# Optimization experiments

Hardware: AMD Instinct MI355X
Metric: run time of the kernel (lower is better)

The kernel has to match this reference:

```python
import jax, jax.numpy as jnp
import numpy as np

N, E = 50000, 1600000
F_IN, F_EDGE, HID = 128, 16, 64
SLOPE = 0.2
EPS_BN = 1e-5


def setup_inputs() -> dict:
    key = jax.random.key(0)
    ks = jax.random.split(key, 24)
    g = lambda k, shp, s=0.1: (jax.random.normal(k, shp, dtype=jnp.float32) * s)
    inp = {
        'x': jax.random.normal(ks[0], (N, F_IN), dtype=jnp.float32),
        'edge_index': jax.random.randint(ks[1], (2, E), 0, N, dtype=jnp.int64),
        'edge_attr': jax.random.normal(ks[2], (E, F_EDGE), dtype=jnp.float32),
        # conv1: F_IN -> HID, 4 heads, concat
        'W1': g(ks[3], (F_IN, 4 * HID)), 'a1s': g(ks[4], (4, HID)), 'a1d': g(ks[5], (4, HID)), 'b1': jnp.zeros((4 * HID,), jnp.float32),
        # conv2: 4*HID -> HID, 4 heads, concat
        'W2': g(ks[6], (4 * HID, 4 * HID)), 'a2s': g(ks[7], (4, HID)), 'a2d': g(ks[8], (4, HID)), 'b2': jnp.zeros((4 * HID,), jnp.float32),
        # conv3: 4*HID -> HID, 1 head
        'W3': g(ks[9], (4 * HID, HID)), 'a3s': g(ks[10], (1, HID)), 'a3d': g(ks[11], (1, HID)), 'b3': jnp.zeros((HID,), jnp.float32),
        'bn1_g': jnp.ones((4 * HID,), jnp.float32), 'bn1_b': jnp.zeros((4 * HID,), jnp.float32),
        'bn2_g': jnp.ones((4 * HID,), jnp.float32), 'bn2_b': jnp.zeros((4 * HID,), jnp.float32),
        'mlp_W1': g(ks[12], (F_EDGE, HID)), 'mlp_b1': jnp.zeros((HID,), jnp.float32),
        'mlp_W2': g(ks[13], (HID, HID)), 'mlp_b2': jnp.zeros((HID,), jnp.float32),
        'fc_W': g(ks[14], (3 * HID, 1)), 'fc_b': jnp.zeros((1,), jnp.float32),
    }
    return inp


def _gat(x, W, a_s, a_d, b, src, dst, heads, dout):
    n = x.shape[0]
    h = (x @ W).reshape(n, heads, dout)                    # [N,H,D]
    ls = jnp.sum(h * a_s, axis=-1)                         # [N,H]
    ld = jnp.sum(h * a_d, axis=-1)
    logits = jax.nn.leaky_relu(ls[src] + ld[dst], SLOPE)   # [E',H]
    m = jax.ops.segment_max(logits, dst, num_segments=n)
    m = jnp.where(jnp.isfinite(m), m, 0.0)
    p = jnp.exp(logits - m[dst])
    s = jax.ops.segment_sum(p, dst, num_segments=n)
    alpha = p / (s[dst] + 1e-16)                           # segment softmax over in-edges
    out = jax.ops.segment_sum(h[src] * alpha[:, :, None], dst, num_segments=n)
    return out.reshape(n, heads * dout) + b


def _bn(x, g, b):
    mu = jnp.mean(x, axis=0)
    var = jnp.var(x, axis=0)
    return (x - mu) * jax.lax.rsqrt(var + EPS_BN) * g + b


def reference(x, edge_index, edge_attr, W1, a1s, a1d, b1, W2, a2s, a2d, b2,
              W3, a3s, a3d, b3, bn1_g, bn1_b, bn2_g, bn2_b,
              mlp_W1, mlp_b1, mlp_W2, mlp_b2, fc_W, fc_b):
    src0, dst0 = edge_index[0], edge_index[1]
    loop = jnp.arange(x.shape[0], dtype=edge_index.dtype)  # PyG adds self-loops
    src = jnp.concatenate([src0, loop])
    dst = jnp.concatenate([dst0, loop])

    h = _gat(x, W1, a1s, a1d, b1, src, dst, 4, HID)
    h = _bn(jax.nn.elu(h), bn1_g, bn1_b)
    h = _gat(h, W2, a2s, a2d, b2, src, dst, 4, HID)
    h = _bn(jax.nn.elu(h), bn2_g, bn2_b)
    h = _gat(h, W3, a3s, a3d, b3, src, dst, 1, HID)        # [N,HID]

    ef = jax.nn.relu(edge_attr @ mlp_W1 + mlp_b1) @ mlp_W2 + mlp_b2  # [E,HID]
    emb = jnp.concatenate([h[src0], h[dst0], ef], axis=1)  # [E,3*HID]
    return (emb @ fc_W + fc_b).squeeze(-1)
```

## Files before the change

### kernel.cpp

```cpp
#include <hip/hip_runtime.h>
#include <math.h>


#define FIN 128
#define HID 64
#define BIN_SHIFT 8

typedef __bf16 bf16x8 __attribute__((ext_vector_type(8)));
typedef float f32x4 __attribute__((ext_vector_type(4)));

__device__ __forceinline__ unsigned f2bfbits(float f) {
    unsigned u = __float_as_uint(f);
    return (u + 0x7fffu + ((u >> 16) & 1u)) >> 16;
}
__device__ __forceinline__ float bf_lo(unsigned w) { return __uint_as_float(w << 16); }
__device__ __forceinline__ float bf_hi(unsigned w) { return __uint_as_float(w & 0xffff0000u); }
__device__ __forceinline__ float bf1(unsigned short s) { return __uint_as_float(((unsigned)s) << 16); }

__device__ __forceinline__ unsigned fenc(float f) {
    unsigned b = __float_as_uint(f);
    return (b & 0x80000000u) ? ~b : (b | 0x80000000u);
}
__device__ __forceinline__ float fdec(unsigned k) {
    unsigned b = (k & 0x80000000u) ? (k ^ 0x80000000u) : ~k;
    return __uint_as_float(b);
}


__global__ __launch_bounds__(256) void bincount_kernel(const int* __restrict__ ei,
                                                       int* __restrict__ bincnt,
                                                       int E, int Etot) {
    __shared__ int h[256];
    int t = threadIdx.x;
    h[t] = 0;
    __syncthreads();
    int base = blockIdx.x * 4096;
    #pragma unroll
    for (int i = 0; i < 16; ++i) {
        int e = base + i * 256 + t;
        if (e < Etot) {
            int d = (e < E) ? ei[E + e] : (e - E);
            atomicAdd(&h[d >> BIN_SHIFT], 1);
        }
    }
    __syncthreads();
    if (h[t]) atomicAdd(&bincnt[t], h[t]);
}

__global__ void scanbins_kernel(const int* __restrict__ bincnt, int* __restrict__ binptr,
                                int* __restrict__ bincur, int NB, int Etot) {
    __shared__ int buf[256];
    int t = threadIdx.x;
    int v = (t < NB) ? bincnt[t] : 0;
    buf[t] = v;
    __syncthreads();
    for (int o = 1; o < 256; o <<= 1) {
        int y = (t >= o) ? buf[t - o] : 0;
        __syncthreads();
        buf[t] += y;
        __syncthreads();
    }
    int excl = buf[t] - v;
    if (t < NB) {
        binptr[t] = excl;
        bincur[t] = excl;
    }
    if (t == 0) binptr[NB] = Etot;
}

__global__ __launch_bounds__(256) void binscatter_kernel(const int* __restrict__ ei,
                                                         int* __restrict__ bincur,
                                                         int2* __restrict__ binned,
                                                         int E, int Etot) {
    __shared__ int h[256];
    __shared__ int gb[256];
    int t = threadIdx.x;
    h[t] = 0;
    __syncthreads();
    int base = blockIdx.x * 4096;
    #pragma unroll
    for (int i = 0; i < 16; ++i) {
        int e = base + i * 256 + t;
        if (e < Etot) {
            int d = (e < E) ? ei[E + e] : (e - E);
            atomicAdd(&h[d >> BIN_SHIFT], 1);
        }
    }
    __syncthreads();
    int cnt = h[t];
    if (cnt) gb[t] = atomicAdd(&bincur[t], cnt);
    __syncthreads();
    h[t] = 0;
    __syncthreads();
    #pragma unroll
    for (int i = 0; i < 16; ++i) {
        int e = base + i * 256 + t;
        if (e < Etot) {
            int s, d;
            if (e < E) { s = ei[e]; d = ei[E + e]; }
            else       { s = e - E; d = e - E; }
            int b = d >> BIN_SHIFT;
            int pos = gb[b] + atomicAdd(&h[b], 1);
            binned[pos] = make_int2(s, d);
        }
    }
}

__global__ __launch_bounds__(256) void bincsr_kernel(const int2* __restrict__ binned,
                                                     const int* __restrict__ binptr,
                                                     int* __restrict__ row_ptr,
                                                     int* __restrict__ col,
                                                     int N, int Etot) {
    __shared__ int h[256];
    __shared__ int cur[256];
    __shared__ int wsum[4];
    int b = blockIdx.x;
    int t = threadIdx.x;
    int lo = b << BIN_SHIFT;
    h[t] = 0;
    __syncthreads();
    int ebeg = binptr[b], eend = binptr[b + 1];
    for (int i = ebeg + t; i < eend; i += 256) atomicAdd(&h[binned[i].y - lo], 1);
    __syncthreads();
    int v = h[t];
    int lane = t & 63, w = t >> 6;
    int x = v;
    #pragma unroll
    for (int o = 1; o < 64; o <<= 1) {
        int y = __shfl_up(x, o);
        if (lane >= o) x += y;
    }
    if (lane == 63) wsum[w] = x;
    __syncthreads();
    int off = 0;
    #pragma unroll
    for (int i = 0; i < 4; ++i) off += (i < w) ? wsum[i] : 0;
    int excl = ebeg + off + x - v;
    int node = lo + t;
    if (node < N) row_ptr[node] = excl;
    cur[t] = excl;
    if (b == 0 && t == 0) row_ptr[N] = Etot;
    __syncthreads();
    for (int i = ebeg + t; i < eend; i += 256) {
        int2 sd = binned[i];
        int pos = atomicAdd(&cur[sd.y - lo], 1);
        col[pos] = sd.x;
    }
}


__global__ __launch_bounds__(256) void mfma_gemm_kernel(
    const float* __restrict__ X, const float* __restrict__ W,
    unsigned short* __restrict__ Yb, int Nrows, int K, int M,
    const float* __restrict__ scale, const float* __restrict__ shift) {
    __shared__ __align__(16) unsigned short a_lds[128][40];
    __shared__ __align__(16) unsigned short b_lds[64][40];
    const int t = threadIdx.x;
    const int row0 = blockIdx.x * 128;
    const int c0 = blockIdx.y * 64;
    const int w = t >> 6, lane = t & 63;
    const int quad = lane >> 4, mrow = lane & 15;
    f32x4 acc[2][4] = {};
    for (int k0 = 0; k0 < K; k0 += 32) {
        #pragma unroll
        for (int i = 0; i < 4; ++i) {
            int f = i * 256 + t;
            int r = f >> 3, kq = f & 7;
            int grow = row0 + r;
            float4 xv = make_float4(0.f, 0.f, 0.f, 0.f);
            if (grow < Nrows) xv = *(const float4*)(X + (size_t)grow * K + k0 + kq * 4);
            if (scale) {
                float4 sc = *(const float4*)(scale + k0 + kq * 4);
                float4 sh = *(const float4*)(shift + k0 + kq * 4);
                xv.x = fmaf(xv.x, sc.x, sh.x);
                xv.y = fmaf(xv.y, sc.y, sh.y);
                xv.z = fmaf(xv.z, sc.z, sh.z);
                xv.w = fmaf(xv.w, sc.w, sh.w);
            }
            ushort4 pk;
            pk.x = (unsigned short)f2bfbits(xv.x);
            pk.y = (unsigned short)f2bfbits(xv.y);
            pk.z = (unsigned short)f2bfbits(xv.z);
            pk.w = (unsigned short)f2bfbits(xv.w);
            *(ushort4*)&a_lds[r][kq * 4] = pk;
        }
        #pragma unroll
        for (int i = 0; i < 2; ++i) {
            int f = i * 256 + t;
            int kr = f >> 4, cq = f & 15;
            float4 wv = *(const float4*)(W + (size_t)(k0 + kr) * M + c0 + cq * 4);
            b_lds[cq * 4 + 0][kr] = (unsigned short)f2bfbits(wv.x);
            b_lds[cq * 4 + 1][kr] = (unsigned short)f2bfbits(wv.y);
            b_lds[cq * 4 + 2][kr] = (unsigned short)f2bfbits(wv.z);
            b_lds[cq * 4 + 3][kr] = (unsigned short)f2bfbits(wv.w);
        }
        __syncthreads();
        bf16x8 a0 = *(const bf16x8*)&a_lds[w * 32 + mrow][quad * 8];
        bf16x8 a1 = *(const bf16x8*)&a_lds[w * 32 + 16 + mrow][quad * 8];
        #pragma unroll
        for (int c = 0; c < 4; ++c) {
            bf16x8 bf = *(const bf16x8*)&b_lds[c * 16 + mrow][quad * 8];
            acc[0][c] = __builtin_amdgcn_mfma_f32_16x16x32_bf16(a0, bf, acc[0][c], 0, 0, 0);
            acc[1][c] = __builtin_amdgcn_mfma_f32_16x16x32_bf16(a1, bf, acc[1][c], 0, 0, 0);
        }
        __syncthreads();
    }
    #pragma unroll
    for (int i = 0; i < 2; ++i) {
        #pragma unroll
        for (int c = 0; c < 4; ++c) {
            #pragma unroll
            for (int r = 0; r < 4; ++r) {
                int grow = row0 + w * 32 + i * 16 + quad * 4 + r;
                if (grow < Nrows)
                    Yb[(size_t)grow * M + c0 + c * 16 + mrow] =
                        (unsigned short)f2bfbits(acc[i][c][r]);
            }
        }
    }
}


template <int H>
__global__ __launch_bounds__(256) void attn_coef_kernel(
    const unsigned short* __restrict__ hb, const float* __restrict__ as_,
    const float* __restrict__ ad_, float* __restrict__ ls,
    float* __restrict__ ld, unsigned* __restrict__ lsmax_g, int N, int ngroups) {
    __shared__ unsigned lmax_lds[4];
    int t = threadIdx.x;
    if (t < 4) lmax_lds[t] = 0;
    __syncthreads();
    int lane = t & 63;
    float lmax = -3.0e38f;
    for (int g = blockIdx.x; g < ngroups; g += gridDim.x) {
        int n = g * 4 + (t >> 6);
        if (n >= N) continue;
        if (H == 4) {
            uint2 w = *(const uint2*)(hb + (size_t)n * 256 + lane * 4);
            float h0 = bf_lo(w.x), h1 = bf_hi(w.x), h2 = bf_lo(w.y), h3 = bf_hi(w.y);
            int cg = lane * 4;
            float4 av = *(const float4*)(as_ + cg);
            float4 dv = *(const float4*)(ad_ + cg);
            float su = h0 * av.x + h1 * av.y + h2 * av.z + h3 * av.w;
            float sd = h0 * dv.x + h1 * dv.y + h2 * dv.z + h3 * dv.w;
            #pragma unroll
            for (int o = 1; o < 16; o <<= 1) {
                su += __shfl_xor(su, o);
                sd += __shfl_xor(sd, o);
            }
            if ((lane & 15) == 0) {
                int hd = lane >> 4;
                ls[(size_t)n * 4 + hd] = su;
                ld[(size_t)n * 4 + hd] = sd;
            }
            lmax = fmaxf(lmax, su);
        } else {
            float hv = bf1(hb[(size_t)n * 64 + lane]);
            float su = hv * as_[lane];
            float sd = hv * ad_[lane];
            #pragma unroll
            for (int o = 32; o; o >>= 1) {
                su += __shfl_xor(su, o);
                sd += __shfl_xor(sd, o);
            }
            if (lane == 0) {
                ls[n] = su;
                ld[n] = sd;
            }
            lmax = fmaxf(lmax, su);
        }
    }
    unsigned key = fenc(lmax);
    if (H == 4) {
        if ((lane & 15) == 0) atomicMax(&lmax_lds[lane >> 4], key);
    } else {
        if (lane == 0) atomicMax(&lmax_lds[0], key);
    }
    __syncthreads();
    if (t < H) atomicMax(&lsmax_g[t], lmax_lds[t]);
}


__global__ __launch_bounds__(256) void agg4_kernel(
    const unsigned short* __restrict__ hb, const float* __restrict__ ls,
    const float* __restrict__ ld, const int* __restrict__ row_ptr,
    const int* __restrict__ col, const float* __restrict__ bias,
    const unsigned* __restrict__ lsmax_g, float* __restrict__ out, int N) {
    int lane = threadIdx.x & 63;
    int n = blockIdx.x * 4 + (threadIdx.x >> 6);
    if (n >= N) return;
    int beg = row_ptr[n], end = row_ptr[n + 1];
    const int hd = lane >> 4;
    float4 ldn = *(const float4*)(ld + (size_t)n * 4);
    float ldn_h = (hd == 0) ? ldn.x : (hd == 1) ? ldn.y : (hd == 2) ? ldn.z : ldn.w;
    float m_h = fmaxf(0.f, ldn_h + fdec(lsmax_g[hd]));
    const int c0 = lane * 4;
    float psum = 0.f;
    float a0 = 0.f, a1 = 0.f, a2 = 0.f, a3 = 0.f;
    for (int base = beg; base < end; base += 64) {
        int el = base + lane;
        int s_r = (el < end) ? col[el] : 0;
        int cnt = min(64, end - base);
        int j = 0;
        for (; j + 8 <= cnt; j += 8) {
            int s[8];
            float l[8];
            uint2 w[8];
            #pragma unroll
            for (int q = 0; q < 8; ++q) s[q] = __shfl(s_r, j + q);
            #pragma unroll
            for (int q = 0; q < 8; ++q) l[q] = ls[(size_t)s[q] * 4 + hd];
            #pragma unroll
            for (int q = 0; q < 8; ++q) w[q] = *(const uint2*)(hb + (size_t)s[q] * 256 + c0);
            #pragma unroll
            for (int q = 0; q < 8; ++q) {
                float g = l[q] + ldn_h;
                g = fmaxf(g, 0.2f * g);
                float p = __expf(g - m_h);
                psum += p;
                a0 = fmaf(p, bf_lo(w[q].x), a0);
                a1 = fmaf(p, bf_hi(w[q].x), a1);
                a2 = fmaf(p, bf_lo(w[q].y), a2);
                a3 = fmaf(p, bf_hi(w[q].y), a3);
            }
        }
        for (; j < cnt; ++j) {
            int sj = __shfl(s_r, j);
            float lv = ls[(size_t)sj * 4 + hd];
            float gg = lv + ldn_h;
            gg = fmaxf(gg, 0.2f * gg);
            float pv = __expf(gg - m_h);
            psum += pv;
            uint2 w = *(const uint2*)(hb + (size_t)sj * 256 + c0);
            a0 = fmaf(pv, bf_lo(w.x), a0);
            a1 = fmaf(pv, bf_hi(w.x), a1);
            a2 = fmaf(pv, bf_lo(w.y), a2);
            a3 = fmaf(pv, bf_hi(w.y), a3);
        }
    }
    float inv = 1.f / (psum + 1e-16f);
    float4 bv = *(const float4*)(bias + c0);
    float4 o;
    o.x = fmaf(a0, inv, bv.x);
    o.y = fmaf(a1, inv, bv.y);
    o.z = fmaf(a2, inv, bv.z);
    o.w = fmaf(a3, inv, bv.w);
    o.x = (o.x > 0.f) ? o.x : expm1f(o.x);
    o.y = (o.y > 0.f) ? o.y : expm1f(o.y);
    o.z = (o.z > 0.f) ? o.z : expm1f(o.z);
    o.w = (o.w > 0.f) ? o.w : expm1f(o.w);
    *(float4*)(out + (size_t)n * 256 + c0) = o;
}


__global__ __launch_bounds__(256) void agg3_kernel(
    const unsigned short* __restrict__ hb, const float* __restrict__ ls,
    const float* __restrict__ ld, const int* __restrict__ row_ptr,
    const int* __restrict__ col, const float* __restrict__ bias,
    const float* __restrict__ fcW, float* __restrict__ up, float* __restrict__ vp,
    const unsigned* __restrict__ lsmax_g, int N) {
    int lane = threadIdx.x & 63;
    int n = blockIdx.x * 4 + (threadIdx.x >> 6);
    if (n >= N) return;
    int beg = row_ptr[n], end = row_ptr[n + 1];
    float ldn = ld[n];
    float m_h = fmaxf(0.f, ldn + fdec(lsmax_g[0]));
    int g = lane >> 4;
    int li = lane & 15;
    float psum = 0.f;
    float a0 = 0.f, a1 = 0.f, a2 = 0.f, a3 = 0.f;
    for (int j = beg + g; j < end; j += 4) {
        int s = col[j];
        float lg = ls[s] + ldn;
        lg = fmaxf(lg, 0.2f * lg);
        float pv = __expf(lg - m_h);
        psum += pv;
        uint2 w = *(const uint2*)(hb + (size_t)s * 64 + li * 4);
        a0 = fmaf(pv, bf_lo(w.x), a0);
        a1 = fmaf(pv, bf_hi(w.x), a1);
        a2 = fmaf(pv, bf_lo(w.y), a2);
        a3 = fmaf(pv, bf_hi(w.y), a3);
    }
    #pragma unroll
    for (int o = 16; o <= 32; o <<= 1) {
        psum += __shfl_xor(psum, o);
        a0 += __shfl_xor(a0, o);
        a1 += __shfl_xor(a1, o);
        a2 += __shfl_xor(a2, o);
        a3 += __shfl_xor(a3, o);
    }
    float inv = 1.f / (psum + 1e-16f);
    int c = li * 4;
    float v0 = fmaf(a0, inv, bias[c + 0]);
    float v1 = fmaf(a1, inv, bias[c + 1]);
    float v2 = fmaf(a2, inv, bias[c + 2]);
    float v3 = fmaf(a3, inv, bias[c + 3]);
    float pu = v0 * fcW[c] + v1 * fcW[c + 1] + v2 * fcW[c + 2] + v3 * fcW[c + 3];
    float pv2 = v0 * fcW[64 + c] + v1 * fcW[64 + c + 1] + v2 * fcW[64 + c + 2] +
                v3 * fcW[64 + c + 3];
    #pragma unroll
    for (int o = 1; o <= 8; o <<= 1) {
        pu += __shfl_xor(pu, o);
        pv2 += __shfl_xor(pv2, o);
    }
    if (lane == 0) {
        up[n] = pu;
        vp[n] = pv2;
    }
}


__global__ __launch_bounds__(256) void bn_stats_kernel(const float* __restrict__ y,
                                                       float* __restrict__ sums,
                                                       int N) {
    int c = threadIdx.x;
    int r0 = blockIdx.x * 128;
    int rend = min(r0 + 128, N);
    float s = 0.f, s2 = 0.f;
    for (int r = r0; r < rend; ++r) {
        float v = y[(size_t)r * 256 + c];
        s += v;
        s2 += v * v;
    }
    atomicAdd(&sums[c], s);
    atomicAdd(&sums[256 + c], s2);
}

__global__ void bn_finalize_kernel(const float* __restrict__ sums,
                                   const float* __restrict__ g,
                                   const float* __restrict__ b,
                                   float* __restrict__ scale,
                                   float* __restrict__ shift, int N) {
    int c = threadIdx.x;
    float invN = 1.f / (float)N;
    float mu = sums[c] * invN;
    float var = sums[256 + c] * invN - mu * mu;
    float sc = g[c] * rsqrtf(var + 1e-5f);
    scale[c] = sc;
    shift[c] = b[c] - mu * sc;
}


__global__ void prep_kernel(const float* __restrict__ mlpW2,
                            const float* __restrict__ mlpb2,
                            const float* __restrict__ fcW,
                            const float* __restrict__ fcb,
                            float* __restrict__ w2f, float* __restrict__ c2) {
    int j = threadIdx.x;
    float s = 0.f;
    for (int k = 0; k < 64; ++k) s += mlpW2[j * 64 + k] * fcW[128 + k];
    w2f[j] = s;
    if (j == 0) {
        float c = fcb[0];
        for (int k = 0; k < 64; ++k) c += mlpb2[k] * fcW[128 + k];
        c2[0] = c;
    }
}

__global__ __launch_bounds__(256) void edge_out_kernel(
    const int* __restrict__ ei, const float* __restrict__ ea,
    const float* __restrict__ W1, const float* __restrict__ b1,
    const float* __restrict__ w2f, const float* __restrict__ c2p,
    const float* __restrict__ u, const float* __restrict__ v,
    float* __restrict__ out, int E) {
    __shared__ __align__(16) float W1T[64][16];
    __shared__ float w2fl[64];
    __shared__ float b1l[64];
    int t = threadIdx.x;
    for (int p = t; p < 1024; p += 256) {
        int i = p >> 6, j = p & 63;
        W1T[j][i] = W1[i * 64 + j];
    }
    if (t < 64) {
        w2fl[t] = w2f[t];
        b1l[t] = b1[t];
    }
    __syncthreads();
    int base = blockIdx.x * 1024;
    float eav[4][16];
    int sidx[4], didx[4];
    bool ok[4];
    #pragma unroll
    for (int k = 0; k < 4; ++k) {
        int e = base + k * 256 + t;
        ok[k] = e < E;
        int ec = ok[k] ? e : 0;
        sidx[k] = ei[ec];
        didx[k] = ei[E + ec];
        const float4* ear = (const float4*)(ea + (size_t)ec * 16);
        float4 q0 = ear[0], q1 = ear[1], q2 = ear[2], q3 = ear[3];
        eav[k][0] = q0.x;  eav[k][1] = q0.y;  eav[k][2] = q0.z;  eav[k][3] = q0.w;
        eav[k][4] = q1.x;  eav[k][5] = q1.y;  eav[k][6] = q1.z;  eav[k][7] = q1.w;
        eav[k][8] = q2.x;  eav[k][9] = q2.y;  eav[k][10] = q2.z; eav[k][11] = q2.w;
        eav[k][12] = q3.x; eav[k][13] = q3.y; eav[k][14] = q3.z; eav[k][15] = q3.w;
    }
    float acc[4] = {0.f, 0.f, 0.f, 0.f};
    #pragma unroll 4
    for (int j = 0; j < 64; ++j) {
        const float4* wr = (const float4*)&W1T[j][0];
        float4 w0 = wr[0], w1 = wr[1], w2 = wr[2], w3 = wr[3];
        float wrow[16] = {w0.x, w0.y, w0.z, w0.w, w1.x, w1.y, w1.z, w1.w,
                          w2.x, w2.y, w2.z, w2.w, w3.x, w3.y, w3.z, w3.w};
        float bj = b1l[j], wj = w2fl[j];
        #pragma unroll
        for (int k = 0; k < 4; ++k) {
            float s = bj;
            #pragma unroll
            for (int q = 0; q < 16; ++q) s = fmaf(eav[k][q], wrow[q], s);
            s = fmaxf(s, 0.f);
            acc[k] = fmaf(s, wj, acc[k]);
        }
    }
    float cc = c2p[0];
    #pragma unroll
    for (int k = 0; k < 4; ++k) {
        if (ok[k]) {
            int e = base + k * 256 + t;
            out[e] = u[sidx[k]] + v[didx[k]] + acc[k] + cc;
        }
    }
}


extern "C" void kernel_launch(void* const* d_in, const int* in_sizes, int n_in,
                              void* d_out, int out_size, void* d_ws, size_t ws_size,
                              hipStream_t stream) {
    const float* x     = (const float*)d_in[0];
    const int*   ei    = (const int*)d_in[1];
    const float* ea    = (const float*)d_in[2];
    const float* W1    = (const float*)d_in[3];
    const float* a1s   = (const float*)d_in[4];
    const float* a1d   = (const float*)d_in[5];
    const float* b1    = (const float*)d_in[6];
    const float* W2    = (const float*)d_in[7];
    const float* a2s   = (const float*)d_in[8];
    const float* a2d   = (const float*)d_in[9];
    const float* b2    = (const float*)d_in[10];
    const float* W3    = (const float*)d_in[11];
    const float* a3s   = (const float*)d_in[12];
    const float* a3d   = (const float*)d_in[13];
    const float* b3    = (const float*)d_in[14];
    const float* bn1g  = (const float*)d_in[15];
    const float* bn1b  = (const float*)d_in[16];
    const float* bn2g  = (const float*)d_in[17];
    const float* bn2b  = (const float*)d_in[18];
    const float* mlpW1 = (const float*)d_in[19];
    const float* mlpb1 = (const float*)d_in[20];
    const float* mlpW2 = (const float*)d_in[21];
    const float* mlpb2 = (const float*)d_in[22];
    const float* fcW   = (const float*)d_in[23];
    const float* fcb   = (const float*)d_in[24];
    float* out = (float*)d_out;

    const int N = in_sizes[0] / FIN;
    const int E = in_sizes[1] / 2;
    const int Etot = E + N;
    const int NB = (N + 255) >> BIN_SHIFT;

    char* wsb = (char*)d_ws;
    size_t off = 0;
    auto alloc = [&](size_t bytes) {
        void* p = wsb + off;
        off += (bytes + 63) & ~(size_t)63;
        return p;
    };
    unsigned short* hAb = (unsigned short*)alloc((size_t)N * 256 * 2);
    float* hB  = (float*)alloc((size_t)N * 256 * 4);
    unsigned short* h3b = (unsigned short*)alloc((size_t)N * 64 * 2);
    float* lsb = (float*)alloc((size_t)N * 4 * 4);
    float* ldb = (float*)alloc((size_t)N * 4 * 4);
    int* row_ptr = (int*)alloc((size_t)(N + 1) * 4);
    int* colb    = (int*)alloc((size_t)Etot * 4);
    int2* binned = (int2*)alloc((size_t)Etot * 8);
    int* bincnt  = (int*)alloc(256 * 4 + 12 * 4);
    unsigned* lsmax1 = (unsigned*)(bincnt + 256);
    unsigned* lsmax2 = lsmax1 + 4;
    unsigned* lsmax3 = lsmax1 + 8;
    int* binptr  = (int*)alloc((size_t)(NB + 1) * 4);
    int* bincur  = (int*)alloc((size_t)NB * 4);
    float* bnsum   = (float*)alloc(512 * 4);
    float* bnscale = (float*)alloc(256 * 4);
    float* bnshift = (float*)alloc(256 * 4);
    float* ub  = (float*)alloc((size_t)N * 4);
    float* vb  = (float*)alloc((size_t)N * 4);
    float* w2f = (float*)alloc(64 * 4);
    float* c2  = (float*)alloc(16 * 4);
    (void)ws_size; (void)n_in; (void)out_size;

    const int nb4 = (N + 3) / 4;
    const int nch = (Etot + 4095) / 4096;

    hipMemsetAsync(bincnt, 0, (256 + 12) * sizeof(int), stream);
    bincount_kernel<<<nch, 256, 0, stream>>>(ei, bincnt, E, Etot);
    scanbins_kernel<<<1, 256, 0, stream>>>(bincnt, binptr, bincur, NB, Etot);
    binscatter_kernel<<<nch, 256, 0, stream>>>(ei, bincur, binned, E, Etot);
    bincsr_kernel<<<NB, 256, 0, stream>>>(binned, binptr, row_ptr, colb, N, Etot);

    dim3 ggrid((N + 127) / 128, 4);
    dim3 ggrid3((N + 127) / 128, 1);

    mfma_gemm_kernel<<<ggrid, 256, 0, stream>>>(x, W1, hAb, N, 128, 256, nullptr, nullptr);
    attn_coef_kernel<4><<<2048, 256, 0, stream>>>(hAb, a1s, a1d, lsb, ldb, lsmax1, N, nb4);
    agg4_kernel<<<nb4, 256, 0, stream>>>(hAb, lsb, ldb, row_ptr, colb, b1, lsmax1, hB, N);
    hipMemsetAsync(bnsum, 0, 512 * sizeof(float), stream);
    bn_stats_kernel<<<(N + 127) / 128, 256, 0, stream>>>(hB, bnsum, N);
    bn_finalize_kernel<<<1, 256, 0, stream>>>(bnsum, bn1g, bn1b, bnscale, bnshift, N);

    mfma_gemm_kernel<<<ggrid, 256, 0, stream>>>(hB, W2, hAb, N, 256, 256, bnscale, bnshift);
    attn_coef_kernel<4><<<2048, 256, 0, stream>>>(hAb, a2s, a2d, lsb, ldb, lsmax2, N, nb4);
    agg4_kernel<<<nb4, 256, 0, stream>>>(hAb, lsb, ldb, row_ptr, colb, b2, lsmax2, hB, N);
    hipMemsetAsync(bnsum, 0, 512 * sizeof(float), stream);
    bn_stats_kernel<<<(N + 127) / 128, 256, 0, stream>>>(hB, bnsum, N);
    bn_finalize_kernel<<<1, 256, 0, stream>>>(bnsum, bn2g, bn2b, bnscale, bnshift, N);

    mfma_gemm_kernel<<<ggrid3, 256, 0, stream>>>(hB, W3, h3b, N, 256, 64, bnscale, bnshift);
    attn_coef_kernel<1><<<2048, 256, 0, stream>>>(h3b, a3s, a3d, lsb, ldb, lsmax3, N, nb4);
    agg3_kernel<<<nb4, 256, 0, stream>>>(h3b, lsb, ldb, row_ptr, colb, b3,
                                         fcW, ub, vb, lsmax3, N);

    prep_kernel<<<1, 64, 0, stream>>>(mlpW2, mlpb2, fcW, fcb, w2f, c2);
    edge_out_kernel<<<(E + 1023) / 1024, 256, 0, stream>>>(ei, ea, mlpW1, mlpb1, w2f, c2,
                                                           ub, vb, out, E);
}
```

Measured before the change: 866.0 us.

## Fuse attention coefs into GEMM epilogue, BN stats into aggregation, switch to fp16

The attention logit dot products now run in the GEMM epilogue, computed from the accumulators with shuffles, so the separate attn_coef pass is gone. The aggregation kernel becomes persistent and accumulates BN sums and squares in shared memory, which removes the bn_stats pass over hB. BN finalize moves into the next GEMM's prologue, and the prep kernel folds into edge_out. Storage and MFMA switch from bf16 to fp16. This cuts launches and full-tensor reads, at the cost of fp16 range risk and a shallower unroll in the gather loop (8 to 4).

```diff
diff --git a/kernel.cpp b/kernel.cpp
--- a/kernel.cpp
+++ b/kernel.cpp
@@ -1,4 +1,5 @@
 #include <hip/hip_runtime.h>
+#include <hip/hip_fp16.h>
 #include <math.h>
 
 
@@ -6,16 +7,17 @@
 #define HID 64
 #define BIN_SHIFT 8
 
-typedef __bf16 bf16x8 __attribute__((ext_vector_type(8)));
+typedef _Float16 f16x8 __attribute__((ext_vector_type(8)));
 typedef float f32x4 __attribute__((ext_vector_type(4)));
 
-__device__ __forceinline__ unsigned f2bfbits(float f) {
-    unsigned u = __float_as_uint(f);
-    return (u + 0x7fffu + ((u >> 16) & 1u)) >> 16;
-}
-__device__ __forceinline__ float bf_lo(unsigned w) { return __uint_as_float(w << 16); }
-__device__ __forceinline__ float bf_hi(unsigned w) { return __uint_as_float(w & 0xffff0000u); }
-__device__ __forceinline__ float bf1(unsigned short s) { return __uint_as_float(((unsigned)s) << 16); }
+__device__ __forceinline__ unsigned short f2hbits(float f) {
+    __half h = __float2half(f);
+    return *reinterpret_cast<unsigned short*>(&h);
+}
+__device__ __forceinline__ float2 hpair(unsigned w) {
+    __half2 h = *reinterpret_cast<__half2*>(&w);
+    return __half22float2(h);
+}
 
 __device__ __forceinline__ unsigned fenc(float f) {
     unsigned b = __float_as_uint(f);
@@ -151,15 +153,32 @@
 
 __global__ __launch_bounds__(256) void mfma_gemm_kernel(
     const float* __restrict__ X, const float* __restrict__ W,
-    unsigned short* __restrict__ Yb, int Nrows, int K, int M,
-    const float* __restrict__ scale, const float* __restrict__ shift) {
+    unsigned short* __restrict__ Yh, int Nrows, int K, int M,
+    const float* __restrict__ bnsum, const float* __restrict__ bng,
+    const float* __restrict__ bnb, float invN,
+    const float* __restrict__ as_, const float* __restrict__ ad_,
+    float* __restrict__ ls, float* __restrict__ ld,
+    unsigned* __restrict__ lsmax_g, int H) {
     __shared__ __align__(16) unsigned short a_lds[128][40];
     __shared__ __align__(16) unsigned short b_lds[64][40];
+    __shared__ __align__(16) float scale_l[256];
+    __shared__ __align__(16) float shift_l[256];
+    __shared__ unsigned lmax_l;
     const int t = threadIdx.x;
     const int row0 = blockIdx.x * 128;
-    const int c0 = blockIdx.y * 64;
+    const int by = blockIdx.y;
+    const int c0 = by * 64;
     const int w = t >> 6, lane = t & 63;
     const int quad = lane >> 4, mrow = lane & 15;
+    if (t == 0) lmax_l = 0;
+    if (bnsum && t < 256) {
+        float mu = bnsum[t] * invN;
+        float var = bnsum[256 + t] * invN - mu * mu;
+        float sc = bng[t] * rsqrtf(var + 1e-5f);
+        scale_l[t] = sc;
+        shift_l[t] = bnb[t] - mu * sc;
+    }
+    __syncthreads();
     f32x4 acc[2][4] = {};
     for (int k0 = 0; k0 < K; k0 += 32) {
         #pragma unroll
@@ -169,19 +188,19 @@
             int grow = row0 + r;
             float4 xv = make_float4(0.f, 0.f, 0.f, 0.f);
             if (grow < Nrows) xv = *(const float4*)(X + (size_t)grow * K + k0 + kq * 4);
-            if (scale) {
-                float4 sc = *(const float4*)(scale + k0 + kq * 4);
-                float4 sh = *(const float4*)(shift + k0 + kq * 4);
+            if (bnsum) {
+                float4 sc = *(const float4*)&scale_l[k0 + kq * 4];
+                float4 sh = *(const float4*)&shift_l[k0 + kq * 4];
                 xv.x = fmaf(xv.x, sc.x, sh.x);
                 xv.y = fmaf(xv.y, sc.y, sh.y);
                 xv.z = fmaf(xv.z, sc.z, sh.z);
                 xv.w = fmaf(xv.w, sc.w, sh.w);
             }
             ushort4 pk;
-            pk.x = (unsigned short)f2bfbits(xv.x);
-            pk.y = (unsigned short)f2bfbits(xv.y);
-            pk.z = (unsigned short)f2bfbits(xv.z);
-            pk.w = (unsigned short)f2bfbits(xv.w);
+            pk.x = f2hbits(xv.x);
+            pk.y = f2hbits(xv.y);
+            pk.z = f2hbits(xv.z);
+            pk.w = f2hbits(xv.w);
             *(ushort4*)&a_lds[r][kq * 4] = pk;
         }
         #pragma unroll
@@ -189,19 +208,19 @@
             int f = i * 256 + t;
             int kr = f >> 4, cq = f & 15;
             float4 wv = *(const float4*)(W + (size_t)(k0 + kr) * M + c0 + cq * 4);
-            b_lds[cq * 4 + 0][kr] = (unsigned short)f2bfbits(wv.x);
-            b_lds[cq * 4 + 1][kr] = (unsigned short)f2bfbits(wv.y);
-            b_lds[cq * 4 + 2][kr] = (unsigned short)f2bfbits(wv.z);
-            b_lds[cq * 4 + 3][kr] = (unsigned short)f2bfbits(wv.w);
+            b_lds[cq * 4 + 0][kr] = f2hbits(wv.x);
+            b_lds[cq * 4 + 1][kr] = f2hbits(wv.y);
+            b_lds[cq * 4 + 2][kr] = f2hbits(wv.z);
+            b_lds[cq * 4 + 3][kr] = f2hbits(wv.w);
         }
         __syncthreads();
-        bf16x8 a0 = *(const bf16x8*)&a_lds[w * 32 + mrow][quad * 8];
-        bf16x8 a1 = *(const bf16x8*)&a_lds[w * 32 + 16 + mrow][quad * 8];
+        f16x8 a0 = *(const f16x8*)&a_lds[w * 32 + mrow][quad * 8];
+        f16x8 a1 = *(const f16x8*)&a_lds[w * 32 + 16 + mrow][quad * 8];
         #pragma unroll
         for (int c = 0; c < 4; ++c) {
-            bf16x8 bf = *(const bf16x8*)&b_lds[c * 16 + mrow][quad * 8];
-            acc[0][c] = __builtin_amdgcn_mfma_f32_16x16x32_bf16(a0, bf, acc[0][c], 0, 0, 0);
-            acc[1][c] = __builtin_amdgcn_mfma_f32_16x16x32_bf16(a1, bf, acc[1][c], 0, 0, 0);
+            f16x8 bf = *(const f16x8*)&b_lds[c * 16 + mrow][quad * 8];
+            acc[0][c] = __builtin_amdgcn_mfma_f32_16x16x32_f16(a0, bf, acc[0][c], 0, 0, 0);
+            acc[1][c] = __builtin_amdgcn_mfma_f32_16x16x32_f16(a1, bf, acc[1][c], 0, 0, 0);
         }
         __syncthreads();
     }
@@ -213,143 +232,145 @@
             for (int r = 0; r < 4; ++r) {
                 int grow = row0 + w * 32 + i * 16 + quad * 4 + r;
                 if (grow < Nrows)
-                    Yb[(size_t)grow * M + c0 + c * 16 + mrow] =
-                        (unsigned short)f2bfbits(acc[i][c][r]);
-            }
-        }
-    }
-}
-
-
-template <int H>
-__global__ __launch_bounds__(256) void attn_coef_kernel(
-    const unsigned short* __restrict__ hb, const float* __restrict__ as_,
-    const float* __restrict__ ad_, float* __restrict__ ls,
-    float* __restrict__ ld, unsigned* __restrict__ lsmax_g, int N, int ngroups) {
-    __shared__ unsigned lmax_lds[4];
-    int t = threadIdx.x;
-    if (t < 4) lmax_lds[t] = 0;
-    __syncthreads();
-    int lane = t & 63;
+                    Yh[(size_t)grow * M + c0 + c * 16 + mrow] = f2hbits(acc[i][c][r]);
+            }
+        }
+    }
+    float asv[4], adv[4];
+    #pragma unroll
+    for (int c = 0; c < 4; ++c) {
+        asv[c] = as_[by * 64 + c * 16 + mrow];
+        adv[c] = ad_[by * 64 + c * 16 + mrow];
+    }
     float lmax = -3.0e38f;
-    for (int g = blockIdx.x; g < ngroups; g += gridDim.x) {
-        int n = g * 4 + (t >> 6);
-        if (n >= N) continue;
-        if (H == 4) {
-            uint2 w = *(const uint2*)(hb + (size_t)n * 256 + lane * 4);
-            float h0 = bf_lo(w.x), h1 = bf_hi(w.x), h2 = bf_lo(w.y), h3 = bf_hi(w.y);
-            int cg = lane * 4;
-            float4 av = *(const float4*)(as_ + cg);
-            float4 dv = *(const float4*)(ad_ + cg);
-            float su = h0 * av.x + h1 * av.y + h2 * av.z + h3 * av.w;
-            float sd = h0 * dv.x + h1 * dv.y + h2 * dv.z + h3 * dv.w;
+    #pragma unroll
+    for (int i = 0; i < 2; ++i) {
+        #pragma unroll
+        for (int r = 0; r < 4; ++r) {
+            float ps = 0.f, pd = 0.f;
             #pragma unroll
-            for (int o = 1; o < 16; o <<= 1) {
-                su += __shfl_xor(su, o);
-                sd += __shfl_xor(sd, o);
-            }
-            if ((lane & 15) == 0) {
-                int hd = lane >> 4;
-                ls[(size_t)n * 4 + hd] = su;
-                ld[(size_t)n * 4 + hd] = sd;
-            }
-            lmax = fmaxf(lmax, su);
-        } else {
-            float hv = bf1(hb[(size_t)n * 64 + lane]);
-            float su = hv * as_[lane];
-            float sd = hv * ad_[lane];
+            for (int c = 0; c < 4; ++c) {
+                ps = fmaf(acc[i][c][r], asv[c], ps);
+                pd = fmaf(acc[i][c][r], adv[c], pd);
+            }
             #pragma unroll
-            for (int o = 32; o; o >>= 1) {
-                su += __shfl_xor(su, o);
-                sd += __shfl_xor(sd, o);
-            }
-            if (lane == 0) {
-                ls[n] = su;
-                ld[n] = sd;
-            }
-            lmax = fmaxf(lmax, su);
-        }
-    }
-    unsigned key = fenc(lmax);
-    if (H == 4) {
-        if ((lane & 15) == 0) atomicMax(&lmax_lds[lane >> 4], key);
-    } else {
-        if (lane == 0) atomicMax(&lmax_lds[0], key);
-    }
-    __syncthreads();
-    if (t < H) atomicMax(&lsmax_g[t], lmax_lds[t]);
-}
-
-
-__global__ __launch_bounds__(256) void agg4_kernel(
+            for (int o = 1; o <= 8; o <<= 1) {
+                ps += __shfl_xor(ps, o);
+                pd += __shfl_xor(pd, o);
+            }
+            int grow = row0 + w * 32 + i * 16 + quad * 4 + r;
+            if (mrow == 0 && grow < Nrows) {
+                ls[(size_t)grow * H + by] = ps;
+                ld[(size_t)grow * H + by] = pd;
+                lmax = fmaxf(lmax, ps);
+            }
+        }
+    }
+    if (mrow == 0) atomicMax(&lmax_l, fenc(lmax));
+    __syncthreads();
+    if (t == 0) atomicMax(&lsmax_g[by], lmax_l);
+}
+
+
+__global__ __launch_bounds__(256) void agg_bn_kernel(
     const unsigned short* __restrict__ hb, const float* __restrict__ ls,
     const float* __restrict__ ld, const int* __restrict__ row_ptr,
     const int* __restrict__ col, const float* __restrict__ bias,
-    const unsigned* __restrict__ lsmax_g, float* __restrict__ out, int N) {
-    int lane = threadIdx.x & 63;
-    int n = blockIdx.x * 4 + (threadIdx.x >> 6);
-    if (n >= N) return;
-    int beg = row_ptr[n], end = row_ptr[n + 1];
+    const unsigned* __restrict__ lsmax_g, float* __restrict__ out,
+    float* __restrict__ bnsum, int N, int ngroups) {
+    __shared__ float accs[4][256];
+    __shared__ float accq[4][256];
+    int t = threadIdx.x;
+    int w = t >> 6, lane = t & 63;
     const int hd = lane >> 4;
-    float4 ldn = *(const float4*)(ld + (size_t)n * 4);
-    float ldn_h = (hd == 0) ? ldn.x : (hd == 1) ? ldn.y : (hd == 2) ? ldn.z : ldn.w;
-    float m_h = fmaxf(0.f, ldn_h + fdec(lsmax_g[hd]));
     const int c0 = lane * 4;
-    float psum = 0.f;
-    float a0 = 0.f, a1 = 0.f, a2 = 0.f, a3 = 0.f;
-    for (int base = beg; base < end; base += 64) {
-        int el = base + lane;
-        int s_r = (el < end) ? col[el] : 0;
-        int cnt = min(64, end - base);
-        int j = 0;
-        for (; j + 8 <= cnt; j += 8) {
-            int s[8];
-            float l[8];
-            uint2 w[8];
-            #pragma unroll
-            for (int q = 0; q < 8; ++q) s[q] = __shfl(s_r, j + q);
-            #pragma unroll
-            for (int q = 0; q < 8; ++q) l[q] = ls[(size_t)s[q] * 4 + hd];
-            #pragma unroll
-            for (int q = 0; q < 8; ++q) w[q] = *(const uint2*)(hb + (size_t)s[q] * 256 + c0);
-            #pragma unroll
-            for (int q = 0; q < 8; ++q) {
-                float g = l[q] + ldn_h;
-                g = fmaxf(g, 0.2f * g);
-                float p = __expf(g - m_h);
-                psum += p;
-                a0 = fmaf(p, bf_lo(w[q].x), a0);
-                a1 = fmaf(p, bf_hi(w[q].x), a1);
-                a2 = fmaf(p, bf_lo(w[q].y), a2);
-                a3 = fmaf(p, bf_hi(w[q].y), a3);
-            }
-        }
-        for (; j < cnt; ++j) {
-            int sj = __shfl(s_r, j);
-            float lv = ls[(size_t)sj * 4 + hd];
-            float gg = lv + ldn_h;
-            gg = fmaxf(gg, 0.2f * gg);
-            float pv = __expf(gg - m_h);
-            psum += pv;
-            uint2 w = *(const uint2*)(hb + (size_t)sj * 256 + c0);
-            a0 = fmaf(pv, bf_lo(w.x), a0);
-            a1 = fmaf(pv, bf_hi(w.x), a1);
-            a2 = fmaf(pv, bf_lo(w.y), a2);
-            a3 = fmaf(pv, bf_hi(w.y), a3);
-        }
-    }
-    float inv = 1.f / (psum + 1e-16f);
-    float4 bv = *(const float4*)(bias + c0);
-    float4 o;
-    o.x = fmaf(a0, inv, bv.x);
-    o.y = fmaf(a1, inv, bv.y);
-    o.z = fmaf(a2, inv, bv.z);
-    o.w = fmaf(a3, inv, bv.w);
-    o.x = (o.x > 0.f) ? o.x : expm1f(o.x);
-    o.y = (o.y > 0.f) ? o.y : expm1f(o.y);
-    o.z = (o.z > 0.f) ? o.z : expm1f(o.z);
-    o.w = (o.w > 0.f) ? o.w : expm1f(o.w);
-    *(float4*)(out + (size_t)n * 256 + c0) = o;
+    #pragma unroll
+    for (int i = 0; i < 4; ++i) {
+        accs[w][c0 + i] = 0.f;
+        accq[w][c0 + i] = 0.f;
+    }
+    float lsm = fdec(lsmax_g[hd]);
+    for (int g = blockIdx.x; g < ngroups; g += gridDim.x) {
+        int n = g * 4 + w;
+        if (n >= N) continue;
+        int beg = row_ptr[n], end = row_ptr[n + 1];
+        float4 ldn = *(const float4*)(ld + (size_t)n * 4);
+        float ldn_h = (hd == 0) ? ldn.x : (hd == 1) ? ldn.y : (hd == 2) ? ldn.z : ldn.w;
+        float m_h = fmaxf(0.f, ldn_h + lsm);
+        float psum = 0.f;
+        float a0 = 0.f, a1 = 0.f, a2 = 0.f, a3 = 0.f;
+        for (int base = beg; base < end; base += 64) {
+            int el = base + lane;
+            int s_r = (el < end) ? col[el] : 0;
+            int cnt = min(64, end - base);
+            int j = 0;
+            for (; j + 4 <= cnt; j += 4) {
+                int s0 = __shfl(s_r, j);
+                int s1 = __shfl(s_r, j + 1);
+                int s2 = __shfl(s_r, j + 2);
+                int s3 = __shfl(s_r, j + 3);
+                float l0 = ls[(size_t)s0 * 4 + hd];
+                float l1 = ls[(size_t)s1 * 4 + hd];
+                float l2 = ls[(size_t)s2 * 4 + hd];
+                float l3 = ls[(size_t)s3 * 4 + hd];
+                uint2 w0 = *(const uint2*)(hb + (size_t)s0 * 256 + c0);
+                uint2 w1 = *(const uint2*)(hb + (size_t)s1 * 256 + c0);
+                uint2 w2 = *(const uint2*)(hb + (size_t)s2 * 256 + c0);
+                uint2 w3 = *(const uint2*)(hb + (size_t)s3 * 256 + c0);
+                float g0 = l0 + ldn_h; g0 = fmaxf(g0, 0.2f * g0);
+                float g1 = l1 + ldn_h; g1 = fmaxf(g1, 0.2f * g1);
+                float g2 = l2 + ldn_h; g2 = fmaxf(g2, 0.2f * g2);
+                float g3 = l3 + ldn_h; g3 = fmaxf(g3, 0.2f * g3);
+                float p0 = __expf(g0 - m_h), p1 = __expf(g1 - m_h);
+                float p2 = __expf(g2 - m_h), p3 = __expf(g3 - m_h);
+                psum += (p0 + p1) + (p2 + p3);
+                float2 f0a = hpair(w0.x), f0b = hpair(w0.y);
+                float2 f1a = hpair(w1.x), f1b = hpair(w1.y);
+                float2 f2a = hpair(w2.x), f2b = hpair(w2.y);
+                float2 f3a = hpair(w3.x), f3b = hpair(w3.y);
+                a0 = fmaf(p0, f0a.x, a0); a1 = fmaf(p0, f0a.y, a1);
+                a2 = fmaf(p0, f0b.x, a2); a3 = fmaf(p0, f0b.y, a3);
+                a0 = fmaf(p1, f1a.x, a0); a1 = fmaf(p1, f1a.y, a1);
+                a2 = fmaf(p1, f1b.x, a2); a3 = fmaf(p1, f1b.y, a3);
+                a0 = fmaf(p2, f2a.x, a0); a1 = fmaf(p2, f2a.y, a1);
+                a2 = fmaf(p2, f2b.x, a2); a3 = fmaf(p2, f2b.y, a3);
+                a0 = fmaf(p3, f3a.x, a0); a1 = fmaf(p3, f3a.y, a1);
+                a2 = fmaf(p3, f3b.x, a2); a3 = fmaf(p3, f3b.y, a3);
+            }
+            for (; j < cnt; ++j) {
+                int sj = __shfl(s_r, j);
+                float lv = ls[(size_t)sj * 4 + hd];
+                float gg = lv + ldn_h; gg = fmaxf(gg, 0.2f * gg);
+                float pv = __expf(gg - m_h);
+                psum += pv;
+                uint2 wj = *(const uint2*)(hb + (size_t)sj * 256 + c0);
+                float2 fa = hpair(wj.x), fb = hpair(wj.y);
+                a0 = fmaf(pv, fa.x, a0); a1 = fmaf(pv, fa.y, a1);
+                a2 = fmaf(pv, fb.x, a2); a3 = fmaf(pv, fb.y, a3);
+            }
+        }
+        float inv = 1.f / (psum + 1e-16f);
+        float4 bv = *(const float4*)(bias + c0);
+        float4 o;
+        o.x = fmaf(a0, inv, bv.x);
+        o.y = fmaf(a1, inv, bv.y);
+        o.z = fmaf(a2, inv, bv.z);
+        o.w = fmaf(a3, inv, bv.w);
+        o.x = (o.x > 0.f) ? o.x : expm1f(o.x);
+        o.y = (o.y > 0.f) ? o.y : expm1f(o.y);
+        o.z = (o.z > 0.f) ? o.z : expm1f(o.z);
+        o.w = (o.w > 0.f) ? o.w : expm1f(o.w);
+        *(float4*)(out + (size_t)n * 256 + c0) = o;
+        accs[w][c0 + 0] += o.x; accq[w][c0 + 0] += o.x * o.x;
+        accs[w][c0 + 1] += o.y; accq[w][c0 + 1] += o.y * o.y;
+        accs[w][c0 + 2] += o.z; accq[w][c0 + 2] += o.z * o.z;
+        accs[w][c0 + 3] += o.w; accq[w][c0 + 3] += o.w * o.w;
+    }
+    __syncthreads();
+    float s = accs[0][t] + accs[1][t] + accs[2][t] + accs[3][t];
+    float q = accq[0][t] + accq[1][t] + accq[2][t] + accq[3][t];
+    atomicAdd(&bnsum[t], s);
+    atomicAdd(&bnsum[256 + t], q);
 }
 
 
@@ -376,10 +397,11 @@
         float pv = __expf(lg - m_h);
         psum += pv;
         uint2 w = *(const uint2*)(hb + (size_t)s * 64 + li * 4);
-        a0 = fmaf(pv, bf_lo(w.x), a0);
-        a1 = fmaf(pv, bf_hi(w.x), a1);
-        a2 = fmaf(pv, bf_lo(w.y), a2);
-        a3 = fmaf(pv, bf_hi(w.y), a3);
+        float2 fa = hpair(w.x), fb = hpair(w.y);
+        a0 = fmaf(pv, fa.x, a0);
+        a1 = fmaf(pv, fa.y, a1);
+        a2 = fmaf(pv, fb.x, a2);
+        a3 = fmaf(pv, fb.y, a3);
     }
     #pragma unroll
     for (int o = 16; o <= 32; o <<= 1) {
@@ -410,70 +432,32 @@
 }
 
 
-__global__ __launch_bounds__(256) void bn_stats_kernel(const float* __restrict__ y,
-                                                       float* __restrict__ sums,
-                                                       int N) {
-    int c = threadIdx.x;
-    int r0 = blockIdx.x * 128;
-    int rend = min(r0 + 128, N);
-    float s = 0.f, s2 = 0.f;
-    for (int r = r0; r < rend; ++r) {
-        float v = y[(size_t)r * 256 + c];
-        s += v;
-        s2 += v * v;
-    }
-    atomicAdd(&sums[c], s);
-    atomicAdd(&sums[256 + c], s2);
-}
-
-__global__ void bn_finalize_kernel(const float* __restrict__ sums,
-                                   const float* __restrict__ g,
-                                   const float* __restrict__ b,
-                                   float* __restrict__ scale,
-                                   float* __restrict__ shift, int N) {
-    int c = threadIdx.x;
-    float invN = 1.f / (float)N;
-    float mu = sums[c] * invN;
-    float var = sums[256 + c] * invN - mu * mu;
-    float sc = g[c] * rsqrtf(var + 1e-5f);
-    scale[c] = sc;
-    shift[c] = b[c] - mu * sc;
-}
-
-
-__global__ void prep_kernel(const float* __restrict__ mlpW2,
-                            const float* __restrict__ mlpb2,
-                            const float* __restrict__ fcW,
-                            const float* __restrict__ fcb,
-                            float* __restrict__ w2f, float* __restrict__ c2) {
-    int j = threadIdx.x;
-    float s = 0.f;
-    for (int k = 0; k < 64; ++k) s += mlpW2[j * 64 + k] * fcW[128 + k];
-    w2f[j] = s;
-    if (j == 0) {
-        float c = fcb[0];
-        for (int k = 0; k < 64; ++k) c += mlpb2[k] * fcW[128 + k];
-        c2[0] = c;
-    }
-}
-
 __global__ __launch_bounds__(256) void edge_out_kernel(
     const int* __restrict__ ei, const float* __restrict__ ea,
     const float* __restrict__ W1, const float* __restrict__ b1,
-    const float* __restrict__ w2f, const float* __restrict__ c2p,
+    const float* __restrict__ mlpW2, const float* __restrict__ mlpb2,
+    const float* __restrict__ fcW, const float* __restrict__ fcb,
     const float* __restrict__ u, const float* __restrict__ v,
     float* __restrict__ out, int E) {
     __shared__ __align__(16) float W1T[64][16];
     __shared__ float w2fl[64];
     __shared__ float b1l[64];
+    __shared__ float c2l;
     int t = threadIdx.x;
     for (int p = t; p < 1024; p += 256) {
         int i = p >> 6, j = p & 63;
         W1T[j][i] = W1[i * 64 + j];
     }
     if (t < 64) {
-        w2fl[t] = w2f[t];
+        float s = 0.f;
+        for (int k = 0; k < 64; ++k) s = fmaf(mlpW2[t * 64 + k], fcW[128 + k], s);
+        w2fl[t] = s;
         b1l[t] = b1[t];
+    }
+    if (t == 0) {
+        float c = fcb[0];
+        for (int k = 0; k < 64; ++k) c = fmaf(mlpb2[k], fcW[128 + k], c);
+        c2l = c;
     }
     __syncthreads();
     int base = blockIdx.x * 1024;
@@ -511,7 +495,7 @@
             acc[k] = fmaf(s, wj, acc[k]);
         }
     }
-    float cc = c2p[0];
+    float cc = c2l;
     #pragma unroll
     for (int k = 0; k < 4; ++k) {
         if (ok[k]) {
@@ -572,25 +556,24 @@
     int* row_ptr = (int*)alloc((size_t)(N + 1) * 4);
     int* colb    = (int*)alloc((size_t)Etot * 4);
     int2* binned = (int2*)alloc((size_t)Etot * 8);
-    int* bincnt  = (int*)alloc(256 * 4 + 12 * 4);
-    unsigned* lsmax1 = (unsigned*)(bincnt + 256);
+    int* zreg    = (int*)alloc((256 + 16 + 512 + 512) * 4);
+    int* bincnt  = zreg;
+    unsigned* lsmax1 = (unsigned*)(zreg + 256);
     unsigned* lsmax2 = lsmax1 + 4;
     unsigned* lsmax3 = lsmax1 + 8;
+    float* bnsumA = (float*)(zreg + 256 + 16);
+    float* bnsumB = bnsumA + 512;
     int* binptr  = (int*)alloc((size_t)(NB + 1) * 4);
     int* bincur  = (int*)alloc((size_t)NB * 4);
-    float* bnsum   = (float*)alloc(512 * 4);
-    float* bnscale = (float*)alloc(256 * 4);
-    float* bnshift = (float*)alloc(256 * 4);
     float* ub  = (float*)alloc((size_t)N * 4);
     float* vb  = (float*)alloc((size_t)N * 4);
-    float* w2f = (float*)alloc(64 * 4);
-    float* c2  = (float*)alloc(16 * 4);
     (void)ws_size; (void)n_in; (void)out_size;
 
     const int nb4 = (N + 3) / 4;
     const int nch = (Etot + 4095) / 4096;
-
-    hipMemsetAsync(bincnt, 0, (256 + 12) * sizeof(int), stream);
+    const float invN = 1.f / (float)N;
+
+    hipMemsetAsync(zreg, 0, (256 + 16 + 512 + 512) * sizeof(int), stream);
     bincount_kernel<<<nch, 256, 0, stream>>>(ei, bincnt, E, Etot);
     scanbins_kernel<<<1, 256, 0, stream>>>(bincnt, binptr, bincur, NB, Etot);
     binscatter_kernel<<<nch, 256, 0, stream>>>(ei, bincur, binned, E, Etot);
@@ -599,26 +582,18 @@
     dim3 ggrid((N + 127) / 128, 4);
     dim3 ggrid3((N + 127) / 128, 1);
 
-    mfma_gemm_kernel<<<ggrid, 256, 0, stream>>>(x, W1, hAb, N, 128, 256, nullptr, nullptr);
-    attn_coef_kernel<4><<<2048, 256, 0, stream>>>(hAb, a1s, a1d, lsb, ldb, lsmax1, N, nb4);
-    agg4_kernel<<<nb4, 256, 0, stream>>>(hAb, lsb, ldb, row_ptr, colb, b1, lsmax1, hB, N);
-    hipMemsetAsync(bnsum, 0, 512 * sizeof(float), stream);
-    bn_stats_kernel<<<(N + 127) / 128, 256, 0, stream>>>(hB, bnsum, N);
-    bn_finalize_kernel<<<1, 256, 0, stream>>>(bnsum, bn1g, bn1b, bnscale, bnshift, N);
-
-    mfma_gemm_kernel<<<ggrid, 256, 0, stream>>>(hB, W2, hAb, N, 256, 256, bnscale, bnshift);
-    attn_coef_kernel<4><<<2048, 256, 0, stream>>>(hAb, a2s, a2d, lsb, ldb, lsmax2, N, nb4);
-    agg4_kernel<<<nb4, 256, 0, stream>>>(hAb, lsb, ldb, row_ptr, colb, b2, lsmax2, hB, N);
-    hipMemsetAsync(bnsum, 0, 512 * sizeof(float), stream);
-    bn_stats_kernel<<<(N + 127) / 128, 256, 0, stream>>>(hB, bnsum, N);
-    bn_finalize_kernel<<<1, 256, 0, stream>>>(bnsum, bn2g, bn2b, bnscale, bnshift, N);
-
-    mfma_gemm_kernel<<<ggrid3, 256, 0, stream>>>(hB, W3, h3b, N, 256, 64, bnscale, bnshift);
-    attn_coef_kernel<1><<<2048, 256, 0, stream>>>(h3b, a3s, a3d, lsb, ldb, lsmax3, N, nb4);
+    mfma_gemm_kernel<<<ggrid, 256, 0, stream>>>(x, W1, hAb, N, 128, 256,
+        nullptr, nullptr, nullptr, invN, a1s, a1d, lsb, ldb, lsmax1, 4);
+    agg_bn_kernel<<<2048, 256, 0, stream>>>(hAb, lsb, ldb, row_ptr, colb, b1,
+                                            lsmax1, hB, bnsumA, N, nb4);
+    mfma_gemm_kernel<<<ggrid, 256, 0, stream>>>(hB, W2, hAb, N, 256, 256,
+        bnsumA, bn1g, bn1b, invN, a2s, a2d, lsb, ldb, lsmax2, 4);
+    agg_bn_kernel<<<2048, 256, 0, stream>>>(hAb, lsb, ldb, row_ptr, colb, b2,
+                                            lsmax2, hB, bnsumB, N, nb4);
+    mfma_gemm_kernel<<<ggrid3, 256, 0, stream>>>(hB, W3, h3b, N, 256, 64,
+        bnsumB, bn2g, bn2b, invN, a3s, a3d, lsb, ldb, lsmax3, 1);
     agg3_kernel<<<nb4, 256, 0, stream>>>(h3b, lsb, ldb, row_ptr, colb, b3,
                                          fcW, ub, vb, lsmax3, N);
-
-    prep_kernel<<<1, 64, 0, stream>>>(mlpW2, mlpb2, fcW, fcb, w2f, c2);
-    edge_out_kernel<<<(E + 1023) / 1024, 256, 0, stream>>>(ei, ea, mlpW1, mlpb1, w2f, c2,
-                                                           ub, vb, out, E);
-}
+    edge_out_kernel<<<(E + 1023) / 1024, 256, 0, stream>>>(
+        ei, ea, mlpW1, mlpb1, mlpW2, mlpb2, fcW, fcb, ub, vb, out, E);
+}
```

After: 784.8 us. -9.4%, faster.
